# Kernel optimization log

Measured on AMD Instinct MI355X. Metric: run time of the kernel, lower is better.

## Reference

```python
import jax, jax.numpy as jnp
import numpy as np

E = 16           # num_experts
D = 4096         # hidden_size
F = 688          # per-expert SwiGLU intermediate size
N = 8192         # total tokens (bsz*seq_len)
CAP_FACTOR = 1.25


def setup_inputs() -> dict:
    key = jax.random.key(0)
    k1, k2, k3, k4, k5, k6 = jax.random.split(key, 6)
    return {
        "x": jax.random.normal(k1, (N, D), dtype=jnp.float32),
        "topk_idx": jax.random.randint(k2, (N,), 0, E, dtype=jnp.int32),
        "topk_scores": jax.random.uniform(k3, (N,), dtype=jnp.float32),
        "Wg": jax.random.normal(k4, (E, D, F), dtype=jnp.float32) * 0.02,
        "Wu": jax.random.normal(k5, (E, D, F), dtype=jnp.float32) * 0.02,
        "Wd": jax.random.normal(k6, (E, F, D), dtype=jnp.float32) * 0.02,
    }


def reference(x, topk_idx, topk_scores, Wg, Wu, Wd):
    # Switch-style top-1 MoE with capacity-based token dropping.
    # Deterministic variant: tokens beyond capacity are dropped in token order
    # (original uses randperm; the math pattern is identical).
    n, d = x.shape
    e = Wg.shape[0]
    cap = int(CAP_FACTOR * n / e)  # static under jit

    # position of each token within its assigned expert (0-based)
    oh = jax.nn.one_hot(topk_idx, e, dtype=jnp.int32)            # [N, E]
    pos = jnp.take_along_axis(jnp.cumsum(oh, axis=0) - 1,
                              topk_idx[:, None].astype(jnp.int32), axis=1)[:, 0]
    keep = pos < cap                                             # [N] bool

    # dispatch: scatter kept tokens into [E, cap, D]; dropped go to dummy row E
    e_safe = jnp.where(keep, topk_idx, e)
    p_safe = jnp.minimum(pos, cap - 1)
    buf = jnp.zeros((e + 1, cap, d), x.dtype).at[e_safe, p_safe].set(x)[:e]

    # per-expert SwiGLU FFN: down(silu(gate(x)) * up(x))
    h = jax.nn.silu(jnp.einsum('ecd,edf->ecf', buf, Wg)) \
        * jnp.einsum('ecd,edf->ecf', buf, Wu)                    # [E, cap, F]
    out = jnp.einsum('ecf,efd->ecd', h, Wd)                      # [E, cap, D]

    # combine: gather back, zero-pad dropped tokens, scale by gate scores
    y = out[topk_idx, p_safe] * keep[:, None].astype(x.dtype)
    y = y * topk_scores[:, None]
    return y
```

## Files before the change

### kernel.cpp

```cpp
#include <hip/hip_runtime.h>
#include <hip/hip_bf16.h>

#define E_ 16
#define D_ 4096
#define F_ 688
#define N_ 8192
#define CAP_ 640

typedef __attribute__((ext_vector_type(8))) short bf16x8;
typedef __attribute__((ext_vector_type(4))) float f32x4;
typedef __attribute__((ext_vector_type(4))) float fvec4;
typedef __attribute__((ext_vector_type(4))) unsigned short usvec4;
typedef __attribute__((ext_vector_type(8))) unsigned short usvec8;

__device__ __forceinline__ unsigned short f2bf(float f) {
    __hip_bfloat16 h = __float2bfloat16(f);
    return __builtin_bit_cast(unsigned short, h);
}

__global__ void k_dispatch(const int* __restrict__ idx,
                           int* __restrict__ slot_token,
                           int* __restrict__ row_of,
                           int* __restrict__ cnt) {
    __shared__ int hist[256][E_];
    const int t = threadIdx.x;
#pragma unroll
    for (int e = 0; e < E_; e++) hist[t][e] = 0;
    __syncthreads();
    const int base = t * (N_ / 256);
    for (int j = 0; j < N_ / 256; j++) {
        int e = idx[base + j];
        hist[t][e]++;
    }
    __syncthreads();
    if (t < E_) {
        int run = 0;
        for (int i = 0; i < 256; i++) { int v = hist[i][t]; hist[i][t] = run; run += v; }
        cnt[t] = run < CAP_ ? run : CAP_;
    }
    for (int s = t; s < E_ * CAP_; s += 256) slot_token[s] = -1;
    __syncthreads();
    for (int j = 0; j < N_ / 256; j++) {
        int i = base + j;
        int e = idx[i];
        int p = hist[t][e]++;
        if (p < CAP_) { slot_token[e * CAP_ + p] = i; row_of[i] = e * CAP_ + p; }
        else          { row_of[i] = -1; }
    }
}

__global__ void k_zero_dropped(const int* __restrict__ row_of, float* __restrict__ y) {
    const int i = blockIdx.x;
    if (row_of[i] >= 0) return;
    fvec4* yp = (fvec4*)(y + (size_t)i * D_);
    fvec4 z = {0.f, 0.f, 0.f, 0.f};
    for (int c = threadIdx.x; c < D_ / 4; c += 256) yp[c] = z;
}

__global__ void k_gather(const float* __restrict__ x, const int* __restrict__ slot_token,
                         unsigned short* __restrict__ Abuf) {
    const int slot = blockIdx.x;
    const int t = slot_token[slot];
    usvec8* dst = (usvec8*)(Abuf + (size_t)slot * D_);
    if (t < 0) {
        usvec8 z = {0, 0, 0, 0, 0, 0, 0, 0};
        for (int c = threadIdx.x; c < D_ / 8; c += 256) dst[c] = z;
    } else {
        const fvec4* src = (const fvec4*)(x + (size_t)t * D_);
        for (int c = threadIdx.x; c < D_ / 8; c += 256) {
            fvec4 a = src[2 * c], b = src[2 * c + 1];
            usvec8 p = {f2bf(a[0]), f2bf(a[1]), f2bf(a[2]), f2bf(a[3]),
                        f2bf(b[0]), f2bf(b[1]), f2bf(b[2]), f2bf(b[3])};
            dst[c] = p;
        }
    }
}

template <bool PRE>
__global__ __launch_bounds__(256, 4) void k_gemm1(
    const float* __restrict__ x, const unsigned short* __restrict__ Abuf,
    const float* __restrict__ Wg, const float* __restrict__ Wu,
    const int* __restrict__ slot_token, const int* __restrict__ cnt,
    unsigned short* __restrict__ H) {
    const int bid = blockIdx.x;
    const int xcd = bid & 7;
    const int j = bid >> 3;
    const int mb = j % 5;
    const int gl = j / 5;
    const int group = xcd * 22 + gl;
    const int e = group / 11, fidx = group % 11;
    const int m0 = mb * 128, f0 = fidx * 64;
    if (m0 >= cnt[e]) return;

    __shared__ __align__(16) unsigned short As[128 * 72];
    __shared__ __align__(16) unsigned short Bgs[64 * 72];
    __shared__ __align__(16) unsigned short Bus[64 * 72];
    __shared__ int tokS[128];

    const int tid = threadIdx.x;
    const int lane = tid & 63, wave = tid >> 6;
    const int wm = wave >> 1, wn = wave & 1;

    if (!PRE && tid < 128) tokS[tid] = slot_token[e * CAP_ + m0 + tid];
    if (!PRE) __syncthreads();

    f32x4 accG[4][2], accU[4][2];
#pragma unroll
    for (int a = 0; a < 4; a++)
#pragma unroll
        for (int b = 0; b < 2; b++) {
            f32x4 z = {0.f, 0.f, 0.f, 0.f};
            accG[a][b] = z; accU[a][b] = z;
        }

    const int f4 = tid & 15, dq = tid >> 4;
    const int fb = f4 * 4, dd = dq * 4;
    const int gcol = f0 + fb;
    const bool bval = gcol < F_;
    const float* WgE = Wg + (size_t)e * D_ * F_;
    const float* WuE = Wu + (size_t)e * D_ * F_;
    const unsigned short* Ae = Abuf + (size_t)(e * CAP_ + m0) * D_;

    for (int kc = 0; kc < D_; kc += 64) {
        if (PRE) {
            const int arow = tid >> 1;
            const int ak0 = (tid & 1) * 32;
#pragma unroll
            for (int s = 0; s < 4; s++) {
                int k = ak0 + s * 8;
                *(usvec8*)&As[arow * 72 + k] = *(const usvec8*)&Ae[(size_t)arow * D_ + kc + k];
            }
        } else {
            const int arow = tid >> 2, akq = tid & 3;
#pragma unroll
            for (int rep = 0; rep < 2; rep++) {
                int row = arow + rep * 64;
                int t = tokS[row];
                const float* src = x + (size_t)(t < 0 ? 0 : t) * D_ + kc;
#pragma unroll
                for (int s = 0; s < 4; s++) {
                    int k = akq * 4 + s * 16;
                    fvec4 v = {0.f, 0.f, 0.f, 0.f};
                    if (t >= 0) v = *(const fvec4*)(src + k);
                    usvec4 p = {f2bf(v[0]), f2bf(v[1]), f2bf(v[2]), f2bf(v[3])};
                    *(usvec4*)&As[row * 72 + k] = p;
                }
            }
        }
        {
            fvec4 vg[4], vu[4];
#pragma unroll
            for (int r = 0; r < 4; r++) {
                fvec4 zg = {0.f, 0.f, 0.f, 0.f};
                vg[r] = zg; vu[r] = zg;
                if (bval) {
                    size_t off = (size_t)(kc + dd + r) * F_ + gcol;
                    vg[r] = *(const fvec4*)(WgE + off);
                    vu[r] = *(const fvec4*)(WuE + off);
                }
            }
#pragma unroll
            for (int i = 0; i < 4; i++) {
                usvec4 pg = {f2bf(vg[0][i]), f2bf(vg[1][i]), f2bf(vg[2][i]), f2bf(vg[3][i])};
                usvec4 pu = {f2bf(vu[0][i]), f2bf(vu[1][i]), f2bf(vu[2][i]), f2bf(vu[3][i])};
                *(usvec4*)&Bgs[(fb + i) * 72 + dd] = pg;
                *(usvec4*)&Bus[(fb + i) * 72 + dd] = pu;
            }
        }
        __syncthreads();
#pragma unroll
        for (int kk = 0; kk < 64; kk += 32) {
            bf16x8 a[4], bg[2], bu[2];
#pragma unroll
            for (int mi = 0; mi < 4; mi++)
                a[mi] = *(const bf16x8*)&As[(wm * 64 + mi * 16 + (lane & 15)) * 72 + kk + ((lane >> 4) << 3)];
#pragma unroll
            for (int ni = 0; ni < 2; ni++) {
                int off = (wn * 32 + ni * 16 + (lane & 15)) * 72 + kk + ((lane >> 4) << 3);
                bg[ni] = *(const bf16x8*)&Bgs[off];
                bu[ni] = *(const bf16x8*)&Bus[off];
            }
#pragma unroll
            for (int mi = 0; mi < 4; mi++)
#pragma unroll
                for (int ni = 0; ni < 2; ni++) {
                    accG[mi][ni] = __builtin_amdgcn_mfma_f32_16x16x32_bf16(a[mi], bg[ni], accG[mi][ni], 0, 0, 0);
                    accU[mi][ni] = __builtin_amdgcn_mfma_f32_16x16x32_bf16(a[mi], bu[ni], accU[mi][ni], 0, 0, 0);
                }
        }
        __syncthreads();
    }
#pragma unroll
    for (int mi = 0; mi < 4; mi++)
#pragma unroll
        for (int ni = 0; ni < 2; ni++) {
            int f = f0 + wn * 32 + ni * 16 + (lane & 15);
            if (f >= F_) continue;
            int rowb = m0 + wm * 64 + mi * 16 + ((lane >> 4) << 2);
#pragma unroll
            for (int q = 0; q < 4; q++) {
                float g = accG[mi][ni][q], u = accU[mi][ni][q];
                float h = g * u / (1.f + __expf(-g));
                H[(size_t)(e * CAP_ + rowb + q) * F_ + f] = f2bf(h);
            }
        }
}

__global__ __launch_bounds__(256, 4) void k_gemm2(
    const unsigned short* __restrict__ H, const float* __restrict__ Wd,
    const int* __restrict__ slot_token, const int* __restrict__ cnt,
    const float* __restrict__ scores, float* __restrict__ y) {
    const int bid = blockIdx.x;
    const int xcd = bid & 7;
    const int j = bid >> 3;
    const int mb = j % 5;
    const int gl = j / 5;
    const int group = xcd * 128 + gl;
    const int e = group >> 6, didx = group & 63;
    const int m0 = mb * 128, d0 = didx * 64;
    if (m0 >= cnt[e]) return;

    __shared__ __align__(16) unsigned short As[128 * 72];
    __shared__ __align__(16) unsigned short Bts[64 * 72];
    __shared__ int tokS[128];
    __shared__ float scS[128];

    const int tid = threadIdx.x;
    const int lane = tid & 63, wave = tid >> 6;
    const int wm = wave >> 1, wn = wave & 1;

    if (tid < 128) {
        int t = slot_token[e * CAP_ + m0 + tid];
        tokS[tid] = t;
        scS[tid] = (t >= 0) ? scores[t] : 0.f;
    }
    __syncthreads();

    f32x4 acc[4][2];
#pragma unroll
    for (int a = 0; a < 4; a++)
#pragma unroll
        for (int b = 0; b < 2; b++) {
            f32x4 z = {0.f, 0.f, 0.f, 0.f};
            acc[a][b] = z;
        }

    const int arow = tid >> 2, akq = tid & 3;
    const int f4 = tid & 15, dq = tid >> 4;
    const int fb = f4 * 4, dd = dq * 4;
    const int gcol = d0 + fb;
    const float* WdE = Wd + (size_t)e * F_ * D_;

    for (int kc = 0; kc < 704; kc += 64) {
#pragma unroll
        for (int rep = 0; rep < 2; rep++) {
            int row = arow + rep * 64;
            size_t slot = (size_t)(e * CAP_ + m0 + row);
#pragma unroll
            for (int s = 0; s < 4; s++) {
                int k = akq * 4 + s * 16;
                usvec4 hv = {0, 0, 0, 0};
                if (kc + k < F_) hv = *(const usvec4*)&H[slot * F_ + kc + k];
                *(usvec4*)&As[row * 72 + k] = hv;
            }
        }
        {
            fvec4 vd[4];
#pragma unroll
            for (int r = 0; r < 4; r++) {
                fvec4 z = {0.f, 0.f, 0.f, 0.f};
                vd[r] = z;
                int kr = kc + dd + r;
                if (kr < F_) vd[r] = *(const fvec4*)(WdE + (size_t)kr * D_ + gcol);
            }
#pragma unroll
            for (int i = 0; i < 4; i++) {
                usvec4 pd = {f2bf(vd[0][i]), f2bf(vd[1][i]), f2bf(vd[2][i]), f2bf(vd[3][i])};
                *(usvec4*)&Bts[(fb + i) * 72 + dd] = pd;
            }
        }
        __syncthreads();
#pragma unroll
        for (int kk = 0; kk < 64; kk += 32) {
            bf16x8 a[4], b[2];
#pragma unroll
            for (int mi = 0; mi < 4; mi++)
                a[mi] = *(const bf16x8*)&As[(wm * 64 + mi * 16 + (lane & 15)) * 72 + kk + ((lane >> 4) << 3)];
#pragma unroll
            for (int ni = 0; ni < 2; ni++)
                b[ni] = *(const bf16x8*)&Bts[(wn * 32 + ni * 16 + (lane & 15)) * 72 + kk + ((lane >> 4) << 3)];
#pragma unroll
            for (int mi = 0; mi < 4; mi++)
#pragma unroll
                for (int ni = 0; ni < 2; ni++)
                    acc[mi][ni] = __builtin_amdgcn_mfma_f32_16x16x32_bf16(a[mi], b[ni], acc[mi][ni], 0, 0, 0);
        }
        __syncthreads();
    }
#pragma unroll
    for (int mi = 0; mi < 4; mi++)
#pragma unroll
        for (int ni = 0; ni < 2; ni++) {
            int d = d0 + wn * 32 + ni * 16 + (lane & 15);
            int rowb = wm * 64 + mi * 16 + ((lane >> 4) << 2);
#pragma unroll
            for (int q = 0; q < 4; q++) {
                int row = rowb + q;
                int t = tokS[row];
                if (t >= 0) y[(size_t)t * D_ + d] = acc[mi][ni][q] * scS[row];
            }
        }
}

extern "C" void kernel_launch(void* const* d_in, const int* in_sizes, int n_in,
                              void* d_out, int out_size, void* d_ws, size_t ws_size,
                              hipStream_t stream) {
    const float* x   = (const float*)d_in[0];
    const int*   idx = (const int*)d_in[1];
    const float* sc  = (const float*)d_in[2];
    const float* Wg  = (const float*)d_in[3];
    const float* Wu  = (const float*)d_in[4];
    const float* Wd  = (const float*)d_in[5];
    float* y = (float*)d_out;

    char* ws = (char*)d_ws;
    int* slot_token = (int*)ws;
    int* row_of     = (int*)(ws + 40960);
    int* cnt        = (int*)(ws + 40960 + 32768);
    const size_t hoff = 131072;
    const size_t hbytes = (size_t)E_ * CAP_ * F_ * 2;
    unsigned short* H = (unsigned short*)(ws + hoff);
    const size_t aoff = hoff + hbytes;
    const size_t abytes = (size_t)E_ * CAP_ * D_ * 2;
    unsigned short* Abuf = (unsigned short*)(ws + aoff);
    const bool pre = ws_size >= aoff + abytes;

    k_dispatch<<<1, 256, 0, stream>>>(idx, slot_token, row_of, cnt);
    k_zero_dropped<<<N_, 256, 0, stream>>>(row_of, y);
    if (pre) {
        k_gather<<<E_ * CAP_, 256, 0, stream>>>(x, slot_token, Abuf);
        k_gemm1<true><<<880, 256, 0, stream>>>(x, Abuf, Wg, Wu, slot_token, cnt, H);
    } else {
        k_gemm1<false><<<880, 256, 0, stream>>>(x, Abuf, Wg, Wu, slot_token, cnt, H);
    }
    k_gemm2<<<5120, 256, 0, stream>>>(H, Wd, slot_token, cnt, sc, y);
}
```

Baseline: 482.9 us.

## Register-prefetch next K tile in both GEMMs and swizzle LDS layouts

Both expert GEMM kernels now load the next 64-wide K tile from global memory into registers while MFMAs run on the current tile in shared memory. This is meant to hide global-load latency behind compute. Shared tiles drop row padding in favour of an XOR-swizzled layout to avoid bank conflicts. Weight loads become float2 per thread. The H buffer row stride is padded to 704 so the second GEMM can load A rows without bounds checks. MFMA sections raise wave priority, and launch bounds drop to 3 blocks per SIMD to leave room for the extra registers. Risk: the padded H columns are never written, so they depend on zeroed Wd rows and on the leftover workspace bits not being NaN.

```diff
diff --git a/kernel.cpp b/kernel.cpp
--- a/kernel.cpp
+++ b/kernel.cpp
@@ -4,18 +4,21 @@
 #define E_ 16
 #define D_ 4096
 #define F_ 688
+#define HS_ 704
 #define N_ 8192
 #define CAP_ 640
 
 typedef __attribute__((ext_vector_type(8))) short bf16x8;
 typedef __attribute__((ext_vector_type(4))) float f32x4;
 typedef __attribute__((ext_vector_type(4))) float fvec4;
-typedef __attribute__((ext_vector_type(4))) unsigned short usvec4;
 typedef __attribute__((ext_vector_type(8))) unsigned short usvec8;
 
 __device__ __forceinline__ unsigned short f2bf(float f) {
     __hip_bfloat16 h = __float2bfloat16(f);
     return __builtin_bit_cast(unsigned short, h);
+}
+__device__ __forceinline__ int lidx(int row, int k) {
+    return row * 64 + (((k >> 3) ^ (row & 7)) << 3) + (k & 7);
 }
 
 __global__ void k_dispatch(const int* __restrict__ idx,
@@ -76,8 +79,77 @@
     }
 }
 
+#define G1_LOAD(rA, rG, rU, KC)                                               \
+  {                                                                           \
+    if (PRE) {                                                                \
+      _Pragma("unroll") for (int rep = 0; rep < 2; rep++)                     \
+      _Pragma("unroll") for (int s = 0; s < 2; s++)                           \
+        rA[rep * 2 + s] = *(const usvec8*)&Ae[(size_t)(ar + rep * 64) * D_ + (KC) + ak + s * 8]; \
+    }                                                                         \
+    _Pragma("unroll") for (int r = 0; r < 8; r++) {                           \
+      size_t off = (size_t)((KC) + kq8 + r) * F_ + gf;                        \
+      rG[r] = bvalid ? *(const float2*)(WgE + off) : fz2;                     \
+      rU[r] = bvalid ? *(const float2*)(WuE + off) : fz2;                     \
+    }                                                                         \
+  }
+
+#define G1_STORE(rA, rG, rU, KC)                                              \
+  {                                                                           \
+    if (PRE) {                                                                \
+      _Pragma("unroll") for (int rep = 0; rep < 2; rep++)                     \
+      _Pragma("unroll") for (int s = 0; s < 2; s++)                           \
+        *(usvec8*)&As[lidx(ar + rep * 64, ak + s * 8)] = rA[rep * 2 + s];     \
+    } else {                                                                  \
+      _Pragma("unroll") for (int rep = 0; rep < 2; rep++) {                   \
+        int row = ar + rep * 64;                                              \
+        int t = tokS[row];                                                    \
+        const float* src = x + (size_t)(t < 0 ? 0 : t) * D_ + (KC) + ak;      \
+        fvec4 v0 = {0.f,0.f,0.f,0.f}, v1 = v0, v2 = v0, v3 = v0;              \
+        if (t >= 0) { v0 = *(const fvec4*)src; v1 = *(const fvec4*)(src + 4); \
+                      v2 = *(const fvec4*)(src + 8); v3 = *(const fvec4*)(src + 12); } \
+        usvec8 p0 = {f2bf(v0[0]), f2bf(v0[1]), f2bf(v0[2]), f2bf(v0[3]),      \
+                     f2bf(v1[0]), f2bf(v1[1]), f2bf(v1[2]), f2bf(v1[3])};     \
+        usvec8 p1 = {f2bf(v2[0]), f2bf(v2[1]), f2bf(v2[2]), f2bf(v2[3]),      \
+                     f2bf(v3[0]), f2bf(v3[1]), f2bf(v3[2]), f2bf(v3[3])};     \
+        *(usvec8*)&As[lidx(row, ak)] = p0;                                    \
+        *(usvec8*)&As[lidx(row, ak + 8)] = p1;                                \
+      }                                                                       \
+    }                                                                         \
+    usvec8 pg0, pg1, pu0, pu1;                                                \
+    _Pragma("unroll") for (int r = 0; r < 8; r++) {                           \
+      pg0[r] = (short)f2bf(rG[r].x); pg1[r] = (short)f2bf(rG[r].y);           \
+      pu0[r] = (short)f2bf(rU[r].x); pu1[r] = (short)f2bf(rU[r].y);           \
+    }                                                                         \
+    *(usvec8*)&Bgs[lidx(fpos, kq8)]     = pg0;                                \
+    *(usvec8*)&Bgs[lidx(fpos + 1, kq8)] = pg1;                                \
+    *(usvec8*)&Bus[lidx(fpos, kq8)]     = pu0;                                \
+    *(usvec8*)&Bus[lidx(fpos + 1, kq8)] = pu1;                                \
+  }
+
+#define G1_COMPUTE                                                            \
+  {                                                                           \
+    __builtin_amdgcn_s_setprio(1);                                            \
+    _Pragma("unroll") for (int kk = 0; kk < 64; kk += 32) {                   \
+      const int ko = kk + ((lane >> 4) << 3);                                 \
+      bf16x8 av[4], bgv[2], buv[2];                                           \
+      _Pragma("unroll") for (int mi = 0; mi < 4; mi++)                        \
+        av[mi] = *(const bf16x8*)&As[lidx(wm * 64 + mi * 16 + (lane & 15), ko)]; \
+      _Pragma("unroll") for (int ni = 0; ni < 2; ni++) {                      \
+        int rr = wn * 32 + ni * 16 + (lane & 15);                             \
+        bgv[ni] = *(const bf16x8*)&Bgs[lidx(rr, ko)];                         \
+        buv[ni] = *(const bf16x8*)&Bus[lidx(rr, ko)];                         \
+      }                                                                       \
+      _Pragma("unroll") for (int mi = 0; mi < 4; mi++)                        \
+      _Pragma("unroll") for (int ni = 0; ni < 2; ni++) {                      \
+        accG[mi][ni] = __builtin_amdgcn_mfma_f32_16x16x32_bf16(av[mi], bgv[ni], accG[mi][ni], 0, 0, 0); \
+        accU[mi][ni] = __builtin_amdgcn_mfma_f32_16x16x32_bf16(av[mi], buv[ni], accU[mi][ni], 0, 0, 0); \
+      }                                                                       \
+    }                                                                         \
+    __builtin_amdgcn_s_setprio(0);                                            \
+  }
+
 template <bool PRE>
-__global__ __launch_bounds__(256, 4) void k_gemm1(
+__global__ __launch_bounds__(256, 3) void k_gemm1(
     const float* __restrict__ x, const unsigned short* __restrict__ Abuf,
     const float* __restrict__ Wg, const float* __restrict__ Wu,
     const int* __restrict__ slot_token, const int* __restrict__ cnt,
@@ -92,17 +164,19 @@
     const int m0 = mb * 128, f0 = fidx * 64;
     if (m0 >= cnt[e]) return;
 
-    __shared__ __align__(16) unsigned short As[128 * 72];
-    __shared__ __align__(16) unsigned short Bgs[64 * 72];
-    __shared__ __align__(16) unsigned short Bus[64 * 72];
+    __shared__ __align__(16) unsigned short As[128 * 64];
+    __shared__ __align__(16) unsigned short Bgs[64 * 64];
+    __shared__ __align__(16) unsigned short Bus[64 * 64];
     __shared__ int tokS[128];
 
     const int tid = threadIdx.x;
     const int lane = tid & 63, wave = tid >> 6;
     const int wm = wave >> 1, wn = wave & 1;
 
-    if (!PRE && tid < 128) tokS[tid] = slot_token[e * CAP_ + m0 + tid];
-    if (!PRE) __syncthreads();
+    if (!PRE) {
+        if (tid < 128) tokS[tid] = slot_token[e * CAP_ + m0 + tid];
+        __syncthreads();
+    }
 
     f32x4 accG[4][2], accU[4][2];
 #pragma unroll
@@ -113,83 +187,40 @@
             accG[a][b] = z; accU[a][b] = z;
         }
 
-    const int f4 = tid & 15, dq = tid >> 4;
-    const int fb = f4 * 4, dd = dq * 4;
-    const int gcol = f0 + fb;
-    const bool bval = gcol < F_;
+    const int ar = tid >> 2, ak = (tid & 3) * 16;
+    const int fpos = (tid & 31) * 2, kq8 = (tid >> 5) * 8;
+    const int gf = f0 + fpos;
+    const bool bvalid = gf < F_;
+    const float2 fz2 = {0.f, 0.f};
     const float* WgE = Wg + (size_t)e * D_ * F_;
     const float* WuE = Wu + (size_t)e * D_ * F_;
     const unsigned short* Ae = Abuf + (size_t)(e * CAP_ + m0) * D_;
 
-    for (int kc = 0; kc < D_; kc += 64) {
-        if (PRE) {
-            const int arow = tid >> 1;
-            const int ak0 = (tid & 1) * 32;
-#pragma unroll
-            for (int s = 0; s < 4; s++) {
-                int k = ak0 + s * 8;
-                *(usvec8*)&As[arow * 72 + k] = *(const usvec8*)&Ae[(size_t)arow * D_ + kc + k];
-            }
-        } else {
-            const int arow = tid >> 2, akq = tid & 3;
-#pragma unroll
-            for (int rep = 0; rep < 2; rep++) {
-                int row = arow + rep * 64;
-                int t = tokS[row];
-                const float* src = x + (size_t)(t < 0 ? 0 : t) * D_ + kc;
-#pragma unroll
-                for (int s = 0; s < 4; s++) {
-                    int k = akq * 4 + s * 16;
-                    fvec4 v = {0.f, 0.f, 0.f, 0.f};
-                    if (t >= 0) v = *(const fvec4*)(src + k);
-                    usvec4 p = {f2bf(v[0]), f2bf(v[1]), f2bf(v[2]), f2bf(v[3])};
-                    *(usvec4*)&As[row * 72 + k] = p;
-                }
-            }
-        }
-        {
-            fvec4 vg[4], vu[4];
-#pragma unroll
-            for (int r = 0; r < 4; r++) {
-                fvec4 zg = {0.f, 0.f, 0.f, 0.f};
-                vg[r] = zg; vu[r] = zg;
-                if (bval) {
-                    size_t off = (size_t)(kc + dd + r) * F_ + gcol;
-                    vg[r] = *(const fvec4*)(WgE + off);
-                    vu[r] = *(const fvec4*)(WuE + off);
-                }
-            }
-#pragma unroll
-            for (int i = 0; i < 4; i++) {
-                usvec4 pg = {f2bf(vg[0][i]), f2bf(vg[1][i]), f2bf(vg[2][i]), f2bf(vg[3][i])};
-                usvec4 pu = {f2bf(vu[0][i]), f2bf(vu[1][i]), f2bf(vu[2][i]), f2bf(vu[3][i])};
-                *(usvec4*)&Bgs[(fb + i) * 72 + dd] = pg;
-                *(usvec4*)&Bus[(fb + i) * 72 + dd] = pu;
-            }
-        }
-        __syncthreads();
-#pragma unroll
-        for (int kk = 0; kk < 64; kk += 32) {
-            bf16x8 a[4], bg[2], bu[2];
-#pragma unroll
-            for (int mi = 0; mi < 4; mi++)
-                a[mi] = *(const bf16x8*)&As[(wm * 64 + mi * 16 + (lane & 15)) * 72 + kk + ((lane >> 4) << 3)];
-#pragma unroll
-            for (int ni = 0; ni < 2; ni++) {
-                int off = (wn * 32 + ni * 16 + (lane & 15)) * 72 + kk + ((lane >> 4) << 3);
-                bg[ni] = *(const bf16x8*)&Bgs[off];
-                bu[ni] = *(const bf16x8*)&Bus[off];
-            }
-#pragma unroll
-            for (int mi = 0; mi < 4; mi++)
-#pragma unroll
-                for (int ni = 0; ni < 2; ni++) {
-                    accG[mi][ni] = __builtin_amdgcn_mfma_f32_16x16x32_bf16(a[mi], bg[ni], accG[mi][ni], 0, 0, 0);
-                    accU[mi][ni] = __builtin_amdgcn_mfma_f32_16x16x32_bf16(a[mi], bu[ni], accU[mi][ni], 0, 0, 0);
-                }
-        }
-        __syncthreads();
-    }
+    usvec8 rA0[4], rA1[4];
+    float2 rG0[8], rG1[8], rU0[8], rU1[8];
+
+    G1_LOAD(rA0, rG0, rU0, 0)
+    for (int t = 0; t < 62; t += 2) {
+        G1_STORE(rA0, rG0, rU0, t * 64)
+        __syncthreads();
+        G1_LOAD(rA1, rG1, rU1, (t + 1) * 64)
+        G1_COMPUTE
+        __syncthreads();
+        G1_STORE(rA1, rG1, rU1, (t + 1) * 64)
+        __syncthreads();
+        G1_LOAD(rA0, rG0, rU0, (t + 2) * 64)
+        G1_COMPUTE
+        __syncthreads();
+    }
+    G1_STORE(rA0, rG0, rU0, 62 * 64)
+    __syncthreads();
+    G1_LOAD(rA1, rG1, rU1, 63 * 64)
+    G1_COMPUTE
+    __syncthreads();
+    G1_STORE(rA1, rG1, rU1, 63 * 64)
+    __syncthreads();
+    G1_COMPUTE
+
 #pragma unroll
     for (int mi = 0; mi < 4; mi++)
 #pragma unroll
@@ -201,12 +232,53 @@
             for (int q = 0; q < 4; q++) {
                 float g = accG[mi][ni][q], u = accU[mi][ni][q];
                 float h = g * u / (1.f + __expf(-g));
-                H[(size_t)(e * CAP_ + rowb + q) * F_ + f] = f2bf(h);
+                H[(size_t)(e * CAP_ + rowb + q) * HS_ + f] = f2bf(h);
             }
         }
 }
 
-__global__ __launch_bounds__(256, 4) void k_gemm2(
+#define G2_LOAD(rA, rB, KC)                                                   \
+  {                                                                           \
+    _Pragma("unroll") for (int rep = 0; rep < 2; rep++)                       \
+    _Pragma("unroll") for (int s = 0; s < 2; s++)                             \
+      rA[rep * 2 + s] = *(const usvec8*)&He[(size_t)(ar + rep * 64) * HS_ + (KC) + ak + s * 8]; \
+    _Pragma("unroll") for (int r = 0; r < 8; r++) {                           \
+      int kr = (KC) + kq8 + r;                                                \
+      rB[r] = (kr < F_) ? *(const float2*)(WdE + (size_t)kr * D_ + gd) : fz2; \
+    }                                                                         \
+  }
+
+#define G2_STORE(rA, rB)                                                      \
+  {                                                                           \
+    _Pragma("unroll") for (int rep = 0; rep < 2; rep++)                       \
+    _Pragma("unroll") for (int s = 0; s < 2; s++)                             \
+      *(usvec8*)&As[lidx(ar + rep * 64, ak + s * 8)] = rA[rep * 2 + s];       \
+    usvec8 p0, p1;                                                            \
+    _Pragma("unroll") for (int r = 0; r < 8; r++) {                           \
+      p0[r] = (short)f2bf(rB[r].x); p1[r] = (short)f2bf(rB[r].y);             \
+    }                                                                         \
+    *(usvec8*)&Bts[lidx(dpos, kq8)]     = p0;                                 \
+    *(usvec8*)&Bts[lidx(dpos + 1, kq8)] = p1;                                 \
+  }
+
+#define G2_COMPUTE                                                            \
+  {                                                                           \
+    __builtin_amdgcn_s_setprio(1);                                            \
+    _Pragma("unroll") for (int kk = 0; kk < 64; kk += 32) {                   \
+      const int ko = kk + ((lane >> 4) << 3);                                 \
+      bf16x8 av[4], bv[2];                                                    \
+      _Pragma("unroll") for (int mi = 0; mi < 4; mi++)                        \
+        av[mi] = *(const bf16x8*)&As[lidx(wm * 64 + mi * 16 + (lane & 15), ko)]; \
+      _Pragma("unroll") for (int ni = 0; ni < 2; ni++)                        \
+        bv[ni] = *(const bf16x8*)&Bts[lidx(wn * 32 + ni * 16 + (lane & 15), ko)]; \
+      _Pragma("unroll") for (int mi = 0; mi < 4; mi++)                        \
+      _Pragma("unroll") for (int ni = 0; ni < 2; ni++)                        \
+        acc[mi][ni] = __builtin_amdgcn_mfma_f32_16x16x32_bf16(av[mi], bv[ni], acc[mi][ni], 0, 0, 0); \
+    }                                                                         \
+    __builtin_amdgcn_s_setprio(0);                                            \
+  }
+
+__global__ __launch_bounds__(256, 3) void k_gemm2(
     const unsigned short* __restrict__ H, const float* __restrict__ Wd,
     const int* __restrict__ slot_token, const int* __restrict__ cnt,
     const float* __restrict__ scores, float* __restrict__ y) {
@@ -220,8 +292,8 @@
     const int m0 = mb * 128, d0 = didx * 64;
     if (m0 >= cnt[e]) return;
 
-    __shared__ __align__(16) unsigned short As[128 * 72];
-    __shared__ __align__(16) unsigned short Bts[64 * 72];
+    __shared__ __align__(16) unsigned short As[128 * 64];
+    __shared__ __align__(16) unsigned short Bts[64 * 64];
     __shared__ int tokS[128];
     __shared__ float scS[128];
 
@@ -245,58 +317,33 @@
             acc[a][b] = z;
         }
 
-    const int arow = tid >> 2, akq = tid & 3;
-    const int f4 = tid & 15, dq = tid >> 4;
-    const int fb = f4 * 4, dd = dq * 4;
-    const int gcol = d0 + fb;
+    const int ar = tid >> 2, ak = (tid & 3) * 16;
+    const int dpos = (tid & 31) * 2, kq8 = (tid >> 5) * 8;
+    const int gd = d0 + dpos;
+    const float2 fz2 = {0.f, 0.f};
     const float* WdE = Wd + (size_t)e * F_ * D_;
-
-    for (int kc = 0; kc < 704; kc += 64) {
-#pragma unroll
-        for (int rep = 0; rep < 2; rep++) {
-            int row = arow + rep * 64;
-            size_t slot = (size_t)(e * CAP_ + m0 + row);
-#pragma unroll
-            for (int s = 0; s < 4; s++) {
-                int k = akq * 4 + s * 16;
-                usvec4 hv = {0, 0, 0, 0};
-                if (kc + k < F_) hv = *(const usvec4*)&H[slot * F_ + kc + k];
-                *(usvec4*)&As[row * 72 + k] = hv;
-            }
-        }
-        {
-            fvec4 vd[4];
-#pragma unroll
-            for (int r = 0; r < 4; r++) {
-                fvec4 z = {0.f, 0.f, 0.f, 0.f};
-                vd[r] = z;
-                int kr = kc + dd + r;
-                if (kr < F_) vd[r] = *(const fvec4*)(WdE + (size_t)kr * D_ + gcol);
-            }
-#pragma unroll
-            for (int i = 0; i < 4; i++) {
-                usvec4 pd = {f2bf(vd[0][i]), f2bf(vd[1][i]), f2bf(vd[2][i]), f2bf(vd[3][i])};
-                *(usvec4*)&Bts[(fb + i) * 72 + dd] = pd;
-            }
-        }
-        __syncthreads();
-#pragma unroll
-        for (int kk = 0; kk < 64; kk += 32) {
-            bf16x8 a[4], b[2];
-#pragma unroll
-            for (int mi = 0; mi < 4; mi++)
-                a[mi] = *(const bf16x8*)&As[(wm * 64 + mi * 16 + (lane & 15)) * 72 + kk + ((lane >> 4) << 3)];
-#pragma unroll
-            for (int ni = 0; ni < 2; ni++)
-                b[ni] = *(const bf16x8*)&Bts[(wn * 32 + ni * 16 + (lane & 15)) * 72 + kk + ((lane >> 4) << 3)];
-#pragma unroll
-            for (int mi = 0; mi < 4; mi++)
-#pragma unroll
-                for (int ni = 0; ni < 2; ni++)
-                    acc[mi][ni] = __builtin_amdgcn_mfma_f32_16x16x32_bf16(a[mi], b[ni], acc[mi][ni], 0, 0, 0);
-        }
-        __syncthreads();
-    }
+    const unsigned short* He = H + (size_t)(e * CAP_ + m0) * HS_;
+
+    usvec8 rA0[4], rA1[4];
+    float2 rB0[8], rB1[8];
+
+    G2_LOAD(rA0, rB0, 0)
+    for (int t = 0; t < 10; t += 2) {
+        G2_STORE(rA0, rB0)
+        __syncthreads();
+        G2_LOAD(rA1, rB1, (t + 1) * 64)
+        G2_COMPUTE
+        __syncthreads();
+        G2_STORE(rA1, rB1)
+        __syncthreads();
+        G2_LOAD(rA0, rB0, (t + 2) * 64)
+        G2_COMPUTE
+        __syncthreads();
+    }
+    G2_STORE(rA0, rB0)
+    __syncthreads();
+    G2_COMPUTE
+
 #pragma unroll
     for (int mi = 0; mi < 4; mi++)
 #pragma unroll
@@ -328,7 +375,7 @@
     int* row_of     = (int*)(ws + 40960);
     int* cnt        = (int*)(ws + 40960 + 32768);
     const size_t hoff = 131072;
-    const size_t hbytes = (size_t)E_ * CAP_ * F_ * 2;
+    const size_t hbytes = (size_t)E_ * CAP_ * HS_ * 2;
     unsigned short* H = (unsigned short*)(ws + hoff);
     const size_t aoff = hoff + hbytes;
     const size_t abytes = (size_t)E_ * CAP_ * D_ * 2;
```

Result: slower. 737.4 us (+52.7%).

## Swizzle LDS tiles, halve gemm1 M-tile, pad H stride, raise MFMA priority

Applied to the files above, without the earlier changes.

Replaces the padded LDS layouts (row stride 72) with an XOR-swizzled stride-64 layout in both GEMMs. gemm1's M tile is halved to 64 rows and its grid doubled to 1760 blocks, which raises parallelism but gives less reuse of each B tile. Weight staging now loads float2 pairs and writes 8-wide bf16 vectors. H gets a padded row stride of 704 so gemm2 can use unguarded 16-byte loads. s_setprio is raised around the MFMA section. The pad columns of H are never written; correctness relies on the zeroed Wd rows cancelling them, so garbage NaN or Inf values in the workspace could leak into the output.

```diff
diff --git a/kernel.cpp b/kernel.cpp
--- a/kernel.cpp
+++ b/kernel.cpp
@@ -4,18 +4,21 @@
 #define E_ 16
 #define D_ 4096
 #define F_ 688
+#define HS_ 704
 #define N_ 8192
 #define CAP_ 640
 
 typedef __attribute__((ext_vector_type(8))) short bf16x8;
 typedef __attribute__((ext_vector_type(4))) float f32x4;
 typedef __attribute__((ext_vector_type(4))) float fvec4;
-typedef __attribute__((ext_vector_type(4))) unsigned short usvec4;
 typedef __attribute__((ext_vector_type(8))) unsigned short usvec8;
 
 __device__ __forceinline__ unsigned short f2bf(float f) {
     __hip_bfloat16 h = __float2bfloat16(f);
     return __builtin_bit_cast(unsigned short, h);
+}
+__device__ __forceinline__ int lidx(int row, int k) {
+    return row * 64 + (((k >> 3) ^ (row & 7)) << 3) + (k & 7);
 }
 
 __global__ void k_dispatch(const int* __restrict__ idx,
@@ -85,123 +88,121 @@
     const int bid = blockIdx.x;
     const int xcd = bid & 7;
     const int j = bid >> 3;
-    const int mb = j % 5;
-    const int gl = j / 5;
+    const int mb = j % 10;
+    const int gl = j / 10;
     const int group = xcd * 22 + gl;
     const int e = group / 11, fidx = group % 11;
-    const int m0 = mb * 128, f0 = fidx * 64;
+    const int m0 = mb * 64, f0 = fidx * 64;
     if (m0 >= cnt[e]) return;
 
-    __shared__ __align__(16) unsigned short As[128 * 72];
-    __shared__ __align__(16) unsigned short Bgs[64 * 72];
-    __shared__ __align__(16) unsigned short Bus[64 * 72];
-    __shared__ int tokS[128];
+    __shared__ __align__(16) unsigned short As[64 * 64];
+    __shared__ __align__(16) unsigned short Bgs[64 * 64];
+    __shared__ __align__(16) unsigned short Bus[64 * 64];
+    __shared__ int tokS[64];
 
     const int tid = threadIdx.x;
     const int lane = tid & 63, wave = tid >> 6;
     const int wm = wave >> 1, wn = wave & 1;
 
-    if (!PRE && tid < 128) tokS[tid] = slot_token[e * CAP_ + m0 + tid];
-    if (!PRE) __syncthreads();
-
-    f32x4 accG[4][2], accU[4][2];
-#pragma unroll
-    for (int a = 0; a < 4; a++)
+    if (!PRE) {
+        if (tid < 64) tokS[tid] = slot_token[e * CAP_ + m0 + tid];
+        __syncthreads();
+    }
+
+    f32x4 accG[2][2], accU[2][2];
+#pragma unroll
+    for (int a = 0; a < 2; a++)
 #pragma unroll
         for (int b = 0; b < 2; b++) {
             f32x4 z = {0.f, 0.f, 0.f, 0.f};
             accG[a][b] = z; accU[a][b] = z;
         }
 
-    const int f4 = tid & 15, dq = tid >> 4;
-    const int fb = f4 * 4, dd = dq * 4;
-    const int gcol = f0 + fb;
-    const bool bval = gcol < F_;
+    const int ar = tid >> 2, ak = (tid & 3) * 16;
+    const int fpos = (tid & 31) * 2, kq8 = (tid >> 5) * 8;
+    const int gf = f0 + fpos;
+    const bool bvalid = gf < F_;
+    const float2 fz2 = {0.f, 0.f};
     const float* WgE = Wg + (size_t)e * D_ * F_;
     const float* WuE = Wu + (size_t)e * D_ * F_;
     const unsigned short* Ae = Abuf + (size_t)(e * CAP_ + m0) * D_;
 
     for (int kc = 0; kc < D_; kc += 64) {
         if (PRE) {
-            const int arow = tid >> 1;
-            const int ak0 = (tid & 1) * 32;
-#pragma unroll
-            for (int s = 0; s < 4; s++) {
-                int k = ak0 + s * 8;
-                *(usvec8*)&As[arow * 72 + k] = *(const usvec8*)&Ae[(size_t)arow * D_ + kc + k];
-            }
+#pragma unroll
+            for (int s = 0; s < 2; s++)
+                *(usvec8*)&As[lidx(ar, ak + s * 8)] =
+                    *(const usvec8*)&Ae[(size_t)ar * D_ + kc + ak + s * 8];
         } else {
-            const int arow = tid >> 2, akq = tid & 3;
-#pragma unroll
-            for (int rep = 0; rep < 2; rep++) {
-                int row = arow + rep * 64;
-                int t = tokS[row];
-                const float* src = x + (size_t)(t < 0 ? 0 : t) * D_ + kc;
-#pragma unroll
-                for (int s = 0; s < 4; s++) {
-                    int k = akq * 4 + s * 16;
-                    fvec4 v = {0.f, 0.f, 0.f, 0.f};
-                    if (t >= 0) v = *(const fvec4*)(src + k);
-                    usvec4 p = {f2bf(v[0]), f2bf(v[1]), f2bf(v[2]), f2bf(v[3])};
-                    *(usvec4*)&As[row * 72 + k] = p;
+            int t = tokS[ar];
+            const float* src = x + (size_t)(t < 0 ? 0 : t) * D_ + kc + ak;
+            fvec4 v0 = {0.f,0.f,0.f,0.f}, v1 = v0, v2 = v0, v3 = v0;
+            if (t >= 0) { v0 = *(const fvec4*)src;        v1 = *(const fvec4*)(src + 4);
+                          v2 = *(const fvec4*)(src + 8);  v3 = *(const fvec4*)(src + 12); }
+            usvec8 p0 = {f2bf(v0[0]), f2bf(v0[1]), f2bf(v0[2]), f2bf(v0[3]),
+                         f2bf(v1[0]), f2bf(v1[1]), f2bf(v1[2]), f2bf(v1[3])};
+            usvec8 p1 = {f2bf(v2[0]), f2bf(v2[1]), f2bf(v2[2]), f2bf(v2[3]),
+                         f2bf(v3[0]), f2bf(v3[1]), f2bf(v3[2]), f2bf(v3[3])};
+            *(usvec8*)&As[lidx(ar, ak)] = p0;
+            *(usvec8*)&As[lidx(ar, ak + 8)] = p1;
+        }
+        {
+            float2 g[8], u[8];
+#pragma unroll
+            for (int r = 0; r < 8; r++) {
+                size_t off = (size_t)(kc + kq8 + r) * F_ + gf;
+                g[r] = bvalid ? *(const float2*)(WgE + off) : fz2;
+                u[r] = bvalid ? *(const float2*)(WuE + off) : fz2;
+            }
+            usvec8 pg0, pg1, pu0, pu1;
+#pragma unroll
+            for (int r = 0; r < 8; r++) {
+                pg0[r] = (short)f2bf(g[r].x); pg1[r] = (short)f2bf(g[r].y);
+                pu0[r] = (short)f2bf(u[r].x); pu1[r] = (short)f2bf(u[r].y);
+            }
+            *(usvec8*)&Bgs[lidx(fpos, kq8)]     = pg0;
+            *(usvec8*)&Bgs[lidx(fpos + 1, kq8)] = pg1;
+            *(usvec8*)&Bus[lidx(fpos, kq8)]     = pu0;
+            *(usvec8*)&Bus[lidx(fpos + 1, kq8)] = pu1;
+        }
+        __syncthreads();
+        __builtin_amdgcn_s_setprio(1);
+#pragma unroll
+        for (int kk = 0; kk < 64; kk += 32) {
+            const int ko = kk + ((lane >> 4) << 3);
+            bf16x8 av[2], bgv[2], buv[2];
+#pragma unroll
+            for (int mi = 0; mi < 2; mi++)
+                av[mi] = *(const bf16x8*)&As[lidx(wm * 32 + mi * 16 + (lane & 15), ko)];
+#pragma unroll
+            for (int ni = 0; ni < 2; ni++) {
+                int rr = wn * 32 + ni * 16 + (lane & 15);
+                bgv[ni] = *(const bf16x8*)&Bgs[lidx(rr, ko)];
+                buv[ni] = *(const bf16x8*)&Bus[lidx(rr, ko)];
+            }
+#pragma unroll
+            for (int mi = 0; mi < 2; mi++)
+#pragma unroll
+                for (int ni = 0; ni < 2; ni++) {
+                    accG[mi][ni] = __builtin_amdgcn_mfma_f32_16x16x32_bf16(av[mi], bgv[ni], accG[mi][ni], 0, 0, 0);
+                    accU[mi][ni] = __builtin_amdgcn_mfma_f32_16x16x32_bf16(av[mi], buv[ni], accU[mi][ni], 0, 0, 0);
                 }
-            }
-        }
-        {
-            fvec4 vg[4], vu[4];
-#pragma unroll
-            for (int r = 0; r < 4; r++) {
-                fvec4 zg = {0.f, 0.f, 0.f, 0.f};
-                vg[r] = zg; vu[r] = zg;
-                if (bval) {
-                    size_t off = (size_t)(kc + dd + r) * F_ + gcol;
-                    vg[r] = *(const fvec4*)(WgE + off);
-                    vu[r] = *(const fvec4*)(WuE + off);
-                }
-            }
-#pragma unroll
-            for (int i = 0; i < 4; i++) {
-                usvec4 pg = {f2bf(vg[0][i]), f2bf(vg[1][i]), f2bf(vg[2][i]), f2bf(vg[3][i])};
-                usvec4 pu = {f2bf(vu[0][i]), f2bf(vu[1][i]), f2bf(vu[2][i]), f2bf(vu[3][i])};
-                *(usvec4*)&Bgs[(fb + i) * 72 + dd] = pg;
-                *(usvec4*)&Bus[(fb + i) * 72 + dd] = pu;
-            }
-        }
-        __syncthreads();
-#pragma unroll
-        for (int kk = 0; kk < 64; kk += 32) {
-            bf16x8 a[4], bg[2], bu[2];
-#pragma unroll
-            for (int mi = 0; mi < 4; mi++)
-                a[mi] = *(const bf16x8*)&As[(wm * 64 + mi * 16 + (lane & 15)) * 72 + kk + ((lane >> 4) << 3)];
-#pragma unroll
-            for (int ni = 0; ni < 2; ni++) {
-                int off = (wn * 32 + ni * 16 + (lane & 15)) * 72 + kk + ((lane >> 4) << 3);
-                bg[ni] = *(const bf16x8*)&Bgs[off];
-                bu[ni] = *(const bf16x8*)&Bus[off];
-            }
-#pragma unroll
-            for (int mi = 0; mi < 4; mi++)
-#pragma unroll
-                for (int ni = 0; ni < 2; ni++) {
-                    accG[mi][ni] = __builtin_amdgcn_mfma_f32_16x16x32_bf16(a[mi], bg[ni], accG[mi][ni], 0, 0, 0);
-                    accU[mi][ni] = __builtin_amdgcn_mfma_f32_16x16x32_bf16(a[mi], bu[ni], accU[mi][ni], 0, 0, 0);
-                }
-        }
-        __syncthreads();
-    }
-#pragma unroll
-    for (int mi = 0; mi < 4; mi++)
+        }
+        __builtin_amdgcn_s_setprio(0);
+        __syncthreads();
+    }
+#pragma unroll
+    for (int mi = 0; mi < 2; mi++)
 #pragma unroll
         for (int ni = 0; ni < 2; ni++) {
             int f = f0 + wn * 32 + ni * 16 + (lane & 15);
             if (f >= F_) continue;
-            int rowb = m0 + wm * 64 + mi * 16 + ((lane >> 4) << 2);
+            int rowb = m0 + wm * 32 + mi * 16 + ((lane >> 4) << 2);
 #pragma unroll
             for (int q = 0; q < 4; q++) {
                 float g = accG[mi][ni][q], u = accU[mi][ni][q];
                 float h = g * u / (1.f + __expf(-g));
-                H[(size_t)(e * CAP_ + rowb + q) * F_ + f] = f2bf(h);
+                H[(size_t)(e * CAP_ + rowb + q) * HS_ + f] = f2bf(h);
             }
         }
 }
@@ -220,8 +221,8 @@
     const int m0 = mb * 128, d0 = didx * 64;
     if (m0 >= cnt[e]) return;
 
-    __shared__ __align__(16) unsigned short As[128 * 72];
-    __shared__ __align__(16) unsigned short Bts[64 * 72];
+    __shared__ __align__(16) unsigned short As[128 * 64];
+    __shared__ __align__(16) unsigned short Bts[64 * 64];
     __shared__ int tokS[128];
     __shared__ float scS[128];
 
@@ -245,56 +246,52 @@
             acc[a][b] = z;
         }
 
-    const int arow = tid >> 2, akq = tid & 3;
-    const int f4 = tid & 15, dq = tid >> 4;
-    const int fb = f4 * 4, dd = dq * 4;
-    const int gcol = d0 + fb;
+    const int ar = tid >> 1, ak = (tid & 1) * 32;
+    const int dpos = (tid & 31) * 2, kq8 = (tid >> 5) * 8;
+    const int gd = d0 + dpos;
+    const float2 fz2 = {0.f, 0.f};
     const float* WdE = Wd + (size_t)e * F_ * D_;
+    const unsigned short* He = H + (size_t)(e * CAP_ + m0) * HS_;
 
     for (int kc = 0; kc < 704; kc += 64) {
 #pragma unroll
-        for (int rep = 0; rep < 2; rep++) {
-            int row = arow + rep * 64;
-            size_t slot = (size_t)(e * CAP_ + m0 + row);
-#pragma unroll
-            for (int s = 0; s < 4; s++) {
-                int k = akq * 4 + s * 16;
-                usvec4 hv = {0, 0, 0, 0};
-                if (kc + k < F_) hv = *(const usvec4*)&H[slot * F_ + kc + k];
-                *(usvec4*)&As[row * 72 + k] = hv;
-            }
-        }
+        for (int s = 0; s < 4; s++)
+            *(usvec8*)&As[lidx(ar, ak + s * 8)] =
+                *(const usvec8*)&He[(size_t)ar * HS_ + kc + ak + s * 8];
         {
-            fvec4 vd[4];
-#pragma unroll
-            for (int r = 0; r < 4; r++) {
-                fvec4 z = {0.f, 0.f, 0.f, 0.f};
-                vd[r] = z;
-                int kr = kc + dd + r;
-                if (kr < F_) vd[r] = *(const fvec4*)(WdE + (size_t)kr * D_ + gcol);
-            }
-#pragma unroll
-            for (int i = 0; i < 4; i++) {
-                usvec4 pd = {f2bf(vd[0][i]), f2bf(vd[1][i]), f2bf(vd[2][i]), f2bf(vd[3][i])};
-                *(usvec4*)&Bts[(fb + i) * 72 + dd] = pd;
-            }
-        }
-        __syncthreads();
+            float2 b[8];
+#pragma unroll
+            for (int r = 0; r < 8; r++) {
+                int kr = kc + kq8 + r;
+                b[r] = (kr < F_) ? *(const float2*)(WdE + (size_t)kr * D_ + gd) : fz2;
+            }
+            usvec8 p0, p1;
+#pragma unroll
+            for (int r = 0; r < 8; r++) {
+                p0[r] = (short)f2bf(b[r].x); p1[r] = (short)f2bf(b[r].y);
+            }
+            *(usvec8*)&Bts[lidx(dpos, kq8)]     = p0;
+            *(usvec8*)&Bts[lidx(dpos + 1, kq8)] = p1;
+        }
+        __syncthreads();
+        __builtin_amdgcn_s_setprio(1);
 #pragma unroll
         for (int kk = 0; kk < 64; kk += 32) {
-            bf16x8 a[4], b[2];
+            const int ko = kk + ((lane >> 4) << 3);
+            bf16x8 av[4], bv[2];
 #pragma unroll
             for (int mi = 0; mi < 4; mi++)
-                a[mi] = *(const bf16x8*)&As[(wm * 64 + mi * 16 + (lane & 15)) * 72 + kk + ((lane >> 4) << 3)];
+                av[mi] = *(const bf16x8*)&As[lidx(wm * 64 + mi * 16 + (lane & 15), ko)];
 #pragma unroll
             for (int ni = 0; ni < 2; ni++)
-                b[ni] = *(const bf16x8*)&Bts[(wn * 32 + ni * 16 + (lane & 15)) * 72 + kk + ((lane >> 4) << 3)];
+                bv[ni] = *(const bf16x8*)&Bts[lidx(wn * 32 + ni * 16 + (lane & 15), ko)];
 #pragma unroll
             for (int mi = 0; mi < 4; mi++)
 #pragma unroll
                 for (int ni = 0; ni < 2; ni++)
-                    acc[mi][ni] = __builtin_amdgcn_mfma_f32_16x16x32_bf16(a[mi], b[ni], acc[mi][ni], 0, 0, 0);
-        }
+                    acc[mi][ni] = __builtin_amdgcn_mfma_f32_16x16x32_bf16(av[mi], bv[ni], acc[mi][ni], 0, 0, 0);
+        }
+        __builtin_amdgcn_s_setprio(0);
         __syncthreads();
     }
 #pragma unroll
@@ -328,7 +325,7 @@
     int* row_of     = (int*)(ws + 40960);
     int* cnt        = (int*)(ws + 40960 + 32768);
     const size_t hoff = 131072;
-    const size_t hbytes = (size_t)E_ * CAP_ * F_ * 2;
+    const size_t hbytes = (size_t)E_ * CAP_ * HS_ * 2;
     unsigned short* H = (unsigned short*)(ws + hoff);
     const size_t aoff = hoff + hbytes;
     const size_t abytes = (size_t)E_ * CAP_ * D_ * 2;
@@ -339,9 +336,9 @@
     k_zero_dropped<<<N_, 256, 0, stream>>>(row_of, y);
     if (pre) {
         k_gather<<<E_ * CAP_, 256, 0, stream>>>(x, slot_token, Abuf);
-        k_gemm1<true><<<880, 256, 0, stream>>>(x, Abuf, Wg, Wu, slot_token, cnt, H);
+        k_gemm1<true><<<1760, 256, 0, stream>>>(x, Abuf, Wg, Wu, slot_token, cnt, H);
     } else {
-        k_gemm1<false><<<880, 256, 0, stream>>>(x, Abuf, Wg, Wu, slot_token, cnt, H);
+        k_gemm1<false><<<1760, 256, 0, stream>>>(x, Abuf, Wg, Wu, slot_token, cnt, H);
     }
     k_gemm2<<<5120, 256, 0, stream>>>(H, Wd, slot_token, cnt, sc, y);
 }
```

Result: slower. 548.9 us (+13.7%).
